# Optimization experiments

Hardware: AMD Instinct MI355X
Metric: run time of the kernel (lower is better)

Reference implementation:

```python
import jax, jax.numpy as jnp
import numpy as np

GROUP_SIZE = 128

def dequantize(imatrix, scales, zeros, group_size, out_dtype):
    # repeat group-wise scales/zeros along axis 0 to full weight shape
    rs = jnp.repeat(scales, group_size, axis=0)
    rz = jnp.repeat(zeros, group_size, axis=0)
    return ((imatrix.astype(rs.dtype) - rz.astype(rs.dtype)) * rs).astype(out_dtype)

def setup_inputs() -> dict:
    key = jax.random.key(0)
    ks = jax.random.split(key, 10)
    H, I, G = 4096, 14336, GROUP_SIZE
    B, S = 4, 2048
    x = jax.random.normal(ks[0], (B, S, H), dtype=jnp.float32)
    gate_w = jax.random.randint(ks[1], (H, I), 0, 16, dtype=jnp.int32)
    gate_z = jax.random.randint(ks[2], (H // G, I), 0, 16, dtype=jnp.int32)
    gate_s = jax.random.uniform(ks[3], (H // G, I), dtype=jnp.float32) * 0.01
    up_w = jax.random.randint(ks[4], (H, I), 0, 16, dtype=jnp.int32)
    up_z = jax.random.randint(ks[5], (H // G, I), 0, 16, dtype=jnp.int32)
    up_s = jax.random.uniform(ks[6], (H // G, I), dtype=jnp.float32) * 0.01
    down_w = jax.random.randint(ks[7], (I, H), 0, 16, dtype=jnp.int32)
    down_z = jax.random.randint(ks[8], (I // G, H), 0, 16, dtype=jnp.int32)
    down_s = jax.random.uniform(ks[9], (I // G, H), dtype=jnp.float32) * 0.01
    return {"x": x, "gate_w": gate_w, "gate_z": gate_z, "gate_s": gate_s,
            "up_w": up_w, "up_z": up_z, "up_s": up_s,
            "down_w": down_w, "down_z": down_z, "down_s": down_s}

def reference(x, gate_w, gate_z, gate_s, up_w, up_z, up_s, down_w, down_z, down_s):
    dt = x.dtype
    gate_proj = dequantize(gate_w, gate_s, gate_z, GROUP_SIZE, dt)  # [H, I]
    up_proj = dequantize(up_w, up_s, up_z, GROUP_SIZE, dt)          # [H, I]
    down_proj = dequantize(down_w, down_s, down_z, GROUP_SIZE, dt)  # [I, H]
    gate = jax.nn.silu(jnp.dot(x, gate_proj))  # [B, S, I]
    up = jnp.dot(x, up_proj)                   # [B, S, I]
    return jnp.dot(gate * up, down_proj)       # [B, S, H]
```

## Files before the change

### kernel.cpp

```cpp
#include <hip/hip_runtime.h>
#include <cstdint>
#include <cstddef>

typedef unsigned short u16;
typedef unsigned int u32;
typedef float f32x4 __attribute__((ext_vector_type(4)));
typedef __bf16 bf16x8 __attribute__((ext_vector_type(8)));

__device__ inline u16 f32_to_bf16(float f) {
  u32 u = __float_as_uint(f);
  u = (u + 0x7FFFu + ((u >> 16) & 1u)) >> 16;
  return (u16)u;
}

#define GLD16(src, dst)                                                        \
  __builtin_amdgcn_global_load_lds(                                            \
      (const __attribute__((address_space(1))) u32*)(src),                     \
      (__attribute__((address_space(3))) u32*)(dst), 16, 0, 0)

__device__ inline void stage_tile(const char* gbase, long stride_b, u16* tile,
                                  int tid) {
  const int wave = tid >> 6, lane = tid & 63;
  const int wbase = wave * 4096;
#pragma unroll
  for (int c = 0; c < 4; ++c) {
    const int d = wbase + c * 1024 + lane * 16;
    const int row = d >> 7;
    const int off = d & 127;
    const int kb = off ^ ((row & 7) << 4);
    const char* src = gbase + (long)row * stride_b + kb;
    char* dst = (char*)tile + wbase + c * 1024;
    GLD16(src, dst);
  }
}

__device__ inline bf16x8 frag_ld(const u16* tile, int row, int ks, int p) {
  const int byte = row * 128 + (((ks << 6) + (p << 4)) ^ ((row & 7) << 4));
  return *(const bf16x8*)((const char*)tile + byte);
}

__global__ void k_convert_x(const float* __restrict__ x, u16* __restrict__ o) {
  const long i = (long)blockIdx.x * 256 + threadIdx.x;
  const float4 a = ((const float4*)x)[i * 2];
  const float4 b = ((const float4*)x)[i * 2 + 1];
  uint4 r;
  r.x = (u32)f32_to_bf16(a.x) | ((u32)f32_to_bf16(a.y) << 16);
  r.y = (u32)f32_to_bf16(a.z) | ((u32)f32_to_bf16(a.w) << 16);
  r.z = (u32)f32_to_bf16(b.x) | ((u32)f32_to_bf16(b.y) << 16);
  r.w = (u32)f32_to_bf16(b.z) | ((u32)f32_to_bf16(b.w) << 16);
  ((uint4*)o)[i] = r;
}

__global__ __launch_bounds__(256) void k_dequant(const int* __restrict__ W,
                                                 const int* __restrict__ Z,
                                                 const float* __restrict__ S,
                                                 u16* __restrict__ out, int K,
                                                 int N) {
  __shared__ u16 ldsT[256 * 66];
  const int k0 = blockIdx.x * 64, n0 = blockIdx.y * 256;
  const int t = threadIdx.x;
  const int n4 = t & 63;
  const int kr = t >> 6;
  const int g = k0 >> 7;
  const int nb = n0 + n4 * 4;
  const int4 z4 = *(const int4*)(Z + (size_t)g * N + nb);
  const float4 s4 = *(const float4*)(S + (size_t)g * N + nb);
#pragma unroll
  for (int pass = 0; pass < 16; ++pass) {
    const int kl = kr + pass * 4;
    const int4 w4 = *(const int4*)(W + (size_t)(k0 + kl) * N + nb);
    ldsT[(n4 * 4 + 0) * 66 + kl] = f32_to_bf16((float)(w4.x - z4.x) * s4.x);
    ldsT[(n4 * 4 + 1) * 66 + kl] = f32_to_bf16((float)(w4.y - z4.y) * s4.y);
    ldsT[(n4 * 4 + 2) * 66 + kl] = f32_to_bf16((float)(w4.z - z4.z) * s4.z);
    ldsT[(n4 * 4 + 3) * 66 + kl] = f32_to_bf16((float)(w4.w - z4.w) * s4.w);
  }
  __syncthreads();
#pragma unroll
  for (int pass = 0; pass < 8; ++pass) {
    const int nl = pass * 32 + (t >> 3);
    const int kc = (t & 7) * 8;
    const u16* p = &ldsT[nl * 66 + kc];
    const u32 w0 = *(const u32*)(p + 0);
    const u32 w1 = *(const u32*)(p + 2);
    const u32 w2 = *(const u32*)(p + 4);
    const u32 w3 = *(const u32*)(p + 6);
    *(uint4*)(out + (size_t)(n0 + nl) * K + k0 + kc) =
        make_uint4(w0, w1, w2, w3);
  }
}

__global__ __launch_bounds__(256, 2) void k_gemm_gu(
    const u16* __restrict__ X, const u16* __restrict__ WG,
    const u16* __restrict__ WU, u16* __restrict__ Hout) {
  __shared__ u16 lA[128 * 64], lG[128 * 64], lU[128 * 64];
  const int m0 = blockIdx.x * 128, n0 = blockIdx.y * 128;
  const int tid = threadIdx.x, lane = tid & 63, p = lane >> 4, r16 = lane & 15;
  const int wave = tid >> 6, wr = wave >> 1, wc = wave & 1;

  f32x4 aG[4][4], aU[4][4];
  const f32x4 zero = {0.f, 0.f, 0.f, 0.f};
#pragma unroll
  for (int i = 0; i < 4; ++i)
#pragma unroll
    for (int j = 0; j < 4; ++j) {
      aG[i][j] = zero;
      aU[i][j] = zero;
    }

  const char* xb = (const char*)(X + (size_t)m0 * 4096);
  const char* gb = (const char*)(WG + (size_t)n0 * 4096);
  const char* ub = (const char*)(WU + (size_t)n0 * 4096);

  for (int kt = 0; kt < 64; ++kt) {
    const int kb = kt * 128;
    stage_tile(xb + kb, 8192, lA, tid);
    stage_tile(gb + kb, 8192, lG, tid);
    stage_tile(ub + kb, 8192, lU, tid);
    __syncthreads();
#pragma unroll
    for (int ks = 0; ks < 2; ++ks) {
      bf16x8 af[4], gf[4], uf[4];
#pragma unroll
      for (int i = 0; i < 4; ++i)
        af[i] = frag_ld(lA, wr * 64 + i * 16 + r16, ks, p);
#pragma unroll
      for (int j = 0; j < 4; ++j) {
        gf[j] = frag_ld(lG, wc * 64 + j * 16 + r16, ks, p);
        uf[j] = frag_ld(lU, wc * 64 + j * 16 + r16, ks, p);
      }
#pragma unroll
      for (int i = 0; i < 4; ++i)
#pragma unroll
        for (int j = 0; j < 4; ++j) {
          aG[i][j] = __builtin_amdgcn_mfma_f32_16x16x32_bf16(af[i], gf[j],
                                                             aG[i][j], 0, 0, 0);
          aU[i][j] = __builtin_amdgcn_mfma_f32_16x16x32_bf16(af[i], uf[j],
                                                             aU[i][j], 0, 0, 0);
        }
    }
    __syncthreads();
  }
#pragma unroll
  for (int i = 0; i < 4; ++i) {
    const int row = m0 + wr * 64 + i * 16 + p * 4;
#pragma unroll
    for (int j = 0; j < 4; ++j) {
      const int col = n0 + wc * 64 + j * 16 + r16;
      u16* dst = Hout + (size_t)row * 14336 + col;
#pragma unroll
      for (int r = 0; r < 4; ++r) {
        const float gv = aG[i][j][r], uv = aU[i][j][r];
        const float sv = gv / (1.f + __expf(-gv)) * uv;
        dst[(size_t)r * 14336] = f32_to_bf16(sv);
      }
    }
  }
}

__global__ __launch_bounds__(256, 2) void k_gemm_down(
    const u16* __restrict__ Hin, const u16* __restrict__ WD,
    float* __restrict__ Out) {
  __shared__ u16 lA[128 * 64], lB[128 * 64];
  const int m0 = blockIdx.x * 128, n0 = blockIdx.y * 128;
  const int tid = threadIdx.x, lane = tid & 63, p = lane >> 4, r16 = lane & 15;
  const int wave = tid >> 6, wr = wave >> 1, wc = wave & 1;

  f32x4 acc[4][4];
  const f32x4 zero = {0.f, 0.f, 0.f, 0.f};
#pragma unroll
  for (int i = 0; i < 4; ++i)
#pragma unroll
    for (int j = 0; j < 4; ++j) acc[i][j] = zero;

  const char* ab = (const char*)(Hin + (size_t)m0 * 14336);
  const char* bb = (const char*)(WD + (size_t)n0 * 14336);

  for (int kt = 0; kt < 224; ++kt) {
    const long kb = (long)kt * 128;
    stage_tile(ab + kb, 28672, lA, tid);
    stage_tile(bb + kb, 28672, lB, tid);
    __syncthreads();
#pragma unroll
    for (int ks = 0; ks < 2; ++ks) {
      bf16x8 af[4], bf[4];
#pragma unroll
      for (int i = 0; i < 4; ++i)
        af[i] = frag_ld(lA, wr * 64 + i * 16 + r16, ks, p);
#pragma unroll
      for (int j = 0; j < 4; ++j)
        bf[j] = frag_ld(lB, wc * 64 + j * 16 + r16, ks, p);
#pragma unroll
      for (int i = 0; i < 4; ++i)
#pragma unroll
        for (int j = 0; j < 4; ++j)
          acc[i][j] = __builtin_amdgcn_mfma_f32_16x16x32_bf16(
              af[i], bf[j], acc[i][j], 0, 0, 0);
    }
    __syncthreads();
  }
#pragma unroll
  for (int i = 0; i < 4; ++i) {
    const int row = m0 + wr * 64 + i * 16 + p * 4;
#pragma unroll
    for (int j = 0; j < 4; ++j) {
      const int col = n0 + wc * 64 + j * 16 + r16;
      float* dst = Out + (size_t)row * 4096 + col;
#pragma unroll
      for (int r = 0; r < 4; ++r) dst[(size_t)r * 4096] = acc[i][j][r];
    }
  }
}

__global__ void k_fill(float* o, long n, float v) {
  const long i = (long)blockIdx.x * 256 + threadIdx.x;
  if (i < n) o[i] = v;
}

extern "C" void kernel_launch(void* const* d_in, const int* in_sizes, int n_in,
                              void* d_out, int out_size, void* d_ws,
                              size_t ws_size, hipStream_t stream) {
  const float* x = (const float*)d_in[0];
  const int* gw = (const int*)d_in[1];
  const int* gz = (const int*)d_in[2];
  const float* gs = (const float*)d_in[3];
  const int* uw = (const int*)d_in[4];
  const int* uz = (const int*)d_in[5];
  const float* us = (const float*)d_in[6];
  const int* dw = (const int*)d_in[7];
  const int* dz = (const int*)d_in[8];
  const float* dsc = (const float*)d_in[9];
  float* out = (float*)d_out;

  const size_t NX = 33554432UL, NW = 58720256UL, NH = 117440512UL;
  const size_t need = 2UL * (NX + 3UL * NW + NH);
  if (ws_size < need) {
    k_fill<<<(out_size + 255) / 256, 256, 0, stream>>>(out, out_size, 1.0e6f);
    return;
  }
  u16* wsx = (u16*)d_ws;
  u16* wgq = wsx + NX;
  u16* wuq = wgq + NW;
  u16* wdq = wuq + NW;
  u16* wh = wdq + NW;

  k_convert_x<<<16384, 256, 0, stream>>>(x, wsx);
  dim3 dq1(64, 56);
  k_dequant<<<dq1, 256, 0, stream>>>(gw, gz, gs, wgq, 4096, 14336);
  k_dequant<<<dq1, 256, 0, stream>>>(uw, uz, us, wuq, 4096, 14336);
  dim3 dq2(224, 16);
  k_dequant<<<dq2, 256, 0, stream>>>(dw, dz, dsc, wdq, 14336, 4096);
  dim3 g1(64, 112);
  k_gemm_gu<<<g1, 256, 0, stream>>>(wsx, wgq, wuq, wh);
  dim3 g2(64, 32);
  k_gemm_down<<<g2, 256, 0, stream>>>(wh, wdq, out);
}
```

Baseline: 2.831 ms.

## Pipeline both GEMMs with double-buffered LDS, larger tiles, and 8-wave ping-pong

Rewrites the gate/up and down GEMM kernels to use 512-thread blocks with larger tiles (256x128 and 256x256). The LDS is split into K-halves and double-buffered, with async global-to-LDS loads issued two tiles ahead, so loads overlap MFMA work instead of stalling on a syncthreads each iteration. Barriers and s_setprio interleave the load issue with the MFMA bursts. In exchange there is more LDS per block and more accumulator registers, which may lower occupancy, and the manual vmcnt accounting is fragile.

```diff
diff --git a/kernel.cpp b/kernel.cpp
--- a/kernel.cpp
+++ b/kernel.cpp
@@ -18,25 +18,26 @@
       (const __attribute__((address_space(1))) u32*)(src),                     \
       (__attribute__((address_space(3))) u32*)(dst), 16, 0, 0)
 
-__device__ inline void stage_tile(const char* gbase, long stride_b, u16* tile,
-                                  int tid) {
-  const int wave = tid >> 6, lane = tid & 63;
-  const int wbase = wave * 4096;
-#pragma unroll
-  for (int c = 0; c < 4; ++c) {
-    const int d = wbase + c * 1024 + lane * 16;
-    const int row = d >> 7;
-    const int off = d & 127;
-    const int kb = off ^ ((row & 7) << 4);
-    const char* src = gbase + (long)row * stride_b + kb;
-    char* dst = (char*)tile + wbase + c * 1024;
-    GLD16(src, dst);
-  }
-}
-
-__device__ inline bf16x8 frag_ld(const u16* tile, int row, int ks, int p) {
-  const int byte = row * 128 + (((ks << 6) + (p << 4)) ^ ((row & 7) << 4));
-  return *(const bf16x8*)((const char*)tile + byte);
+#define SBAR() __builtin_amdgcn_s_barrier()
+#define SETPRIO(x) __builtin_amdgcn_s_setprio(x)
+#define WAIT_LGKM0()                                                           \
+  do {                                                                         \
+    asm volatile("s_waitcnt lgkmcnt(0)" ::: "memory");                         \
+    __builtin_amdgcn_sched_barrier(0);                                         \
+  } while (0)
+#define MFMA16(a, b, c) __builtin_amdgcn_mfma_f32_16x16x32_bf16(a, b, c, 0, 0, 0)
+
+__device__ inline void stage_one(const char* laneBase, long colByte,
+                                 long strideB, int rowBase, u16* ldsHalf,
+                                 int wave) {
+  const char* src = laneBase + colByte + (long)rowBase * strideB;
+  char* dst = (char*)ldsHalf + rowBase * 64 + wave * 1024;
+  GLD16(src, dst);
+}
+
+__device__ inline bf16x8 fragK(const u16* half, int row, int p) {
+  const int byte = row * 64 + (((p ^ row) & 3) << 4);
+  return *(const bf16x8*)((const char*)half + byte);
 }
 
 __global__ void k_convert_x(const float* __restrict__ x, u16* __restrict__ o) {
@@ -89,63 +90,110 @@
   }
 }
 
-__global__ __launch_bounds__(256, 2) void k_gemm_gu(
+__global__ __launch_bounds__(512, 2) void k_gemm_gu(
     const u16* __restrict__ X, const u16* __restrict__ WG,
     const u16* __restrict__ WU, u16* __restrict__ Hout) {
-  __shared__ u16 lA[128 * 64], lG[128 * 64], lU[128 * 64];
-  const int m0 = blockIdx.x * 128, n0 = blockIdx.y * 128;
-  const int tid = threadIdx.x, lane = tid & 63, p = lane >> 4, r16 = lane & 15;
-  const int wave = tid >> 6, wr = wave >> 1, wc = wave & 1;
-
-  f32x4 aG[4][4], aU[4][4];
+  __shared__ __align__(16) u16 lA[2][2][8192];
+  __shared__ __align__(16) u16 lG[2][2][4096];
+  __shared__ __align__(16) u16 lU[2][2][4096];
+  const int NKT = 64;
+  const int m0 = blockIdx.x * 256, n0 = blockIdx.y * 128;
+  const int tid = threadIdx.x, lane = tid & 63, wave = tid >> 6;
+  const int p = lane >> 4, r16 = lane & 15;
+  const int wr = wave >> 2, wc = wave & 3;
+
+  const int srow = wave * 16 + (lane >> 2);
+  const int kb = (((lane & 3) ^ (lane >> 2)) & 3) << 4;
+  const char* baA = (const char*)X + (long)(m0 + srow) * 8192 + kb;
+  const char* baG = (const char*)WG + (long)(n0 + srow) * 8192 + kb;
+  const char* baU = (const char*)WU + (long)(n0 + srow) * 8192 + kb;
+
+#define ISS_A(kts, ksh, rb) \
+  stage_one(baA, (long)(kts)*128 + (ksh)*64, 8192, rb, &lA[(kts)&1][ksh][0], wave)
+#define ISS_G(kts, ksh) \
+  stage_one(baG, (long)(kts)*128 + (ksh)*64, 8192, 0, &lG[(kts)&1][ksh][0], wave)
+#define ISS_U(kts, ksh) \
+  stage_one(baU, (long)(kts)*128 + (ksh)*64, 8192, 0, &lU[(kts)&1][ksh][0], wave)
+
+  f32x4 aG[8][2], aU[8][2];
   const f32x4 zero = {0.f, 0.f, 0.f, 0.f};
 #pragma unroll
-  for (int i = 0; i < 4; ++i)
-#pragma unroll
-    for (int j = 0; j < 4; ++j) {
+  for (int i = 0; i < 8; ++i)
+#pragma unroll
+    for (int j = 0; j < 2; ++j) {
       aG[i][j] = zero;
       aU[i][j] = zero;
     }
 
-  const char* xb = (const char*)(X + (size_t)m0 * 4096);
-  const char* gb = (const char*)(WG + (size_t)n0 * 4096);
-  const char* ub = (const char*)(WU + (size_t)n0 * 4096);
-
-  for (int kt = 0; kt < 64; ++kt) {
-    const int kb = kt * 128;
-    stage_tile(xb + kb, 8192, lA, tid);
-    stage_tile(gb + kb, 8192, lG, tid);
-    stage_tile(ub + kb, 8192, lU, tid);
-    __syncthreads();
-#pragma unroll
-    for (int ks = 0; ks < 2; ++ks) {
-      bf16x8 af[4], gf[4], uf[4];
-#pragma unroll
-      for (int i = 0; i < 4; ++i)
-        af[i] = frag_ld(lA, wr * 64 + i * 16 + r16, ks, p);
-#pragma unroll
-      for (int j = 0; j < 4; ++j) {
-        gf[j] = frag_ld(lG, wc * 64 + j * 16 + r16, ks, p);
-        uf[j] = frag_ld(lU, wc * 64 + j * 16 + r16, ks, p);
-      }
-#pragma unroll
-      for (int i = 0; i < 4; ++i)
-#pragma unroll
-        for (int j = 0; j < 4; ++j) {
-          aG[i][j] = __builtin_amdgcn_mfma_f32_16x16x32_bf16(af[i], gf[j],
-                                                             aG[i][j], 0, 0, 0);
-          aU[i][j] = __builtin_amdgcn_mfma_f32_16x16x32_bf16(af[i], uf[j],
-                                                             aU[i][j], 0, 0, 0);
-        }
-    }
-    __syncthreads();
-  }
-#pragma unroll
-  for (int i = 0; i < 4; ++i) {
-    const int row = m0 + wr * 64 + i * 16 + p * 4;
-#pragma unroll
-    for (int j = 0; j < 4; ++j) {
-      const int col = n0 + wc * 64 + j * 16 + r16;
+  ISS_A(0, 0, 0); ISS_A(0, 0, 128); ISS_G(0, 0); ISS_U(0, 0);
+  ISS_A(0, 1, 0); ISS_A(0, 1, 128); ISS_G(0, 1); ISS_U(0, 1);
+  ISS_A(1, 0, 0); ISS_A(1, 0, 128); ISS_G(1, 0); ISS_U(1, 0);
+  ISS_A(1, 1, 0); ISS_A(1, 1, 128);
+  asm volatile("s_waitcnt vmcnt(6)" ::: "memory");
+  SBAR();
+
+  for (int kt = 0; kt < NKT; ++kt) {
+    const int b = kt & 1;
+    const bool g1 = (kt + 1 < NKT), g2 = (kt + 2 < NKT);
+#pragma unroll
+    for (int ksh = 0; ksh < 2; ++ksh) {
+      bf16x8 af[8], gf[2], uf[2];
+      const u16* hA = &lA[b][ksh][0];
+      const u16* hG = &lG[b][ksh][0];
+      const u16* hU = &lU[b][ksh][0];
+#pragma unroll
+      for (int i = 0; i < 8; ++i)
+        af[i] = fragK(hA, wr * 128 + i * 16 + r16, p);
+#pragma unroll
+      for (int j = 0; j < 2; ++j) {
+        gf[j] = fragK(hG, wc * 32 + j * 16 + r16, p);
+        uf[j] = fragK(hU, wc * 32 + j * 16 + r16, p);
+      }
+      if (ksh == 0) {
+        if (g1) { ISS_G(kt + 1, 1); ISS_U(kt + 1, 1); }
+      } else {
+        if (g2) { ISS_G(kt + 2, 0); ISS_U(kt + 2, 0); }
+      }
+      SBAR();
+      WAIT_LGKM0();
+      SETPRIO(1);
+#pragma unroll
+      for (int i = 0; i < 8; ++i)
+#pragma unroll
+        for (int j = 0; j < 2; ++j) aG[i][j] = MFMA16(af[i], gf[j], aG[i][j]);
+      SETPRIO(0);
+      SBAR();
+      if (ksh == 0) {
+        if (g2) { ISS_A(kt + 2, 0, 0); ISS_A(kt + 2, 0, 128); }
+      } else {
+        if (g2) { ISS_A(kt + 2, 1, 0); ISS_A(kt + 2, 1, 128); }
+      }
+      SBAR();
+      SETPRIO(1);
+#pragma unroll
+      for (int i = 0; i < 8; ++i)
+#pragma unroll
+        for (int j = 0; j < 2; ++j) aU[i][j] = MFMA16(af[i], uf[j], aU[i][j]);
+      SETPRIO(0);
+      if (ksh == 1) {
+        if (kt < NKT - 2)
+          asm volatile("s_waitcnt vmcnt(6)" ::: "memory");
+        else if (kt == NKT - 2)
+          asm volatile("s_waitcnt vmcnt(0)" ::: "memory");
+      }
+      SBAR();
+    }
+  }
+#undef ISS_A
+#undef ISS_G
+#undef ISS_U
+
+#pragma unroll
+  for (int i = 0; i < 8; ++i) {
+    const int row = m0 + wr * 128 + i * 16 + p * 4;
+#pragma unroll
+    for (int j = 0; j < 2; ++j) {
+      const int col = n0 + wc * 32 + j * 16 + r16;
       u16* dst = Hout + (size_t)row * 14336 + col;
 #pragma unroll
       for (int r = 0; r < 4; ++r) {
@@ -157,50 +205,98 @@
   }
 }
 
-__global__ __launch_bounds__(256, 2) void k_gemm_down(
+__global__ __launch_bounds__(512, 2) void k_gemm_down(
     const u16* __restrict__ Hin, const u16* __restrict__ WD,
     float* __restrict__ Out) {
-  __shared__ u16 lA[128 * 64], lB[128 * 64];
-  const int m0 = blockIdx.x * 128, n0 = blockIdx.y * 128;
-  const int tid = threadIdx.x, lane = tid & 63, p = lane >> 4, r16 = lane & 15;
-  const int wave = tid >> 6, wr = wave >> 1, wc = wave & 1;
-
-  f32x4 acc[4][4];
+  __shared__ __align__(16) u16 lA[2][2][8192];
+  __shared__ __align__(16) u16 lB[2][2][8192];
+  const int NKT = 224;
+  const int m0 = blockIdx.x * 256, n0 = blockIdx.y * 256;
+  const int tid = threadIdx.x, lane = tid & 63, wave = tid >> 6;
+  const int p = lane >> 4, r16 = lane & 15;
+  const int wr = wave >> 2, wc = wave & 3;
+
+  const int srow = wave * 16 + (lane >> 2);
+  const int kb = (((lane & 3) ^ (lane >> 2)) & 3) << 4;
+  const char* baA = (const char*)Hin + (long)(m0 + srow) * 28672 + kb;
+  const char* baB = (const char*)WD + (long)(n0 + srow) * 28672 + kb;
+
+#define ISS_A(kts, ksh, rb) \
+  stage_one(baA, (long)(kts)*128 + (ksh)*64, 28672, rb, &lA[(kts)&1][ksh][0], wave)
+#define ISS_B(kts, ksh, rb) \
+  stage_one(baB, (long)(kts)*128 + (ksh)*64, 28672, rb, &lB[(kts)&1][ksh][0], wave)
+
+  f32x4 acc[8][4];
   const f32x4 zero = {0.f, 0.f, 0.f, 0.f};
 #pragma unroll
-  for (int i = 0; i < 4; ++i)
+  for (int i = 0; i < 8; ++i)
 #pragma unroll
     for (int j = 0; j < 4; ++j) acc[i][j] = zero;
 
-  const char* ab = (const char*)(Hin + (size_t)m0 * 14336);
-  const char* bb = (const char*)(WD + (size_t)n0 * 14336);
-
-  for (int kt = 0; kt < 224; ++kt) {
-    const long kb = (long)kt * 128;
-    stage_tile(ab + kb, 28672, lA, tid);
-    stage_tile(bb + kb, 28672, lB, tid);
-    __syncthreads();
-#pragma unroll
-    for (int ks = 0; ks < 2; ++ks) {
-      bf16x8 af[4], bf[4];
-#pragma unroll
-      for (int i = 0; i < 4; ++i)
-        af[i] = frag_ld(lA, wr * 64 + i * 16 + r16, ks, p);
+  ISS_A(0, 0, 0); ISS_A(0, 0, 128); ISS_B(0, 0, 0); ISS_B(0, 0, 128);
+  ISS_A(0, 1, 0); ISS_A(0, 1, 128); ISS_B(0, 1, 0); ISS_B(0, 1, 128);
+  ISS_A(1, 0, 0); ISS_A(1, 0, 128); ISS_B(1, 0, 0); ISS_B(1, 0, 128);
+  ISS_A(1, 1, 0); ISS_A(1, 1, 128);
+  asm volatile("s_waitcnt vmcnt(6)" ::: "memory");
+  SBAR();
+
+  for (int kt = 0; kt < NKT; ++kt) {
+    const int b = kt & 1;
+    const bool g1 = (kt + 1 < NKT), g2 = (kt + 2 < NKT);
+#pragma unroll
+    for (int ksh = 0; ksh < 2; ++ksh) {
+      bf16x8 af[8], bfr[4];
+      const u16* hA = &lA[b][ksh][0];
+      const u16* hB = &lB[b][ksh][0];
+#pragma unroll
+      for (int i = 0; i < 8; ++i)
+        af[i] = fragK(hA, wr * 128 + i * 16 + r16, p);
 #pragma unroll
       for (int j = 0; j < 4; ++j)
-        bf[j] = frag_ld(lB, wc * 64 + j * 16 + r16, ks, p);
-#pragma unroll
-      for (int i = 0; i < 4; ++i)
-#pragma unroll
-        for (int j = 0; j < 4; ++j)
-          acc[i][j] = __builtin_amdgcn_mfma_f32_16x16x32_bf16(
-              af[i], bf[j], acc[i][j], 0, 0, 0);
-    }
-    __syncthreads();
-  }
-#pragma unroll
-  for (int i = 0; i < 4; ++i) {
-    const int row = m0 + wr * 64 + i * 16 + p * 4;
+        bfr[j] = fragK(hB, wc * 64 + j * 16 + r16, p);
+      if (ksh == 0) {
+        if (g1) { ISS_B(kt + 1, 1, 0); ISS_B(kt + 1, 1, 128); }
+      } else {
+        if (g2) { ISS_B(kt + 2, 0, 0); ISS_B(kt + 2, 0, 128); }
+      }
+      SBAR();
+      WAIT_LGKM0();
+      SETPRIO(1);
+#pragma unroll
+      for (int i = 0; i < 8; ++i)
+#pragma unroll
+        for (int j = 0; j < 2; ++j)
+          acc[i][j] = MFMA16(af[i], bfr[j], acc[i][j]);
+      SETPRIO(0);
+      SBAR();
+      if (ksh == 0) {
+        if (g2) { ISS_A(kt + 2, 0, 0); ISS_A(kt + 2, 0, 128); }
+      } else {
+        if (g2) { ISS_A(kt + 2, 1, 0); ISS_A(kt + 2, 1, 128); }
+      }
+      SBAR();
+      SETPRIO(1);
+#pragma unroll
+      for (int i = 0; i < 8; ++i)
+#pragma unroll
+        for (int j = 2; j < 4; ++j)
+          acc[i][j] = MFMA16(af[i], bfr[j], acc[i][j]);
+      SETPRIO(0);
+      if (ksh == 1) {
+        if (kt < NKT - 2)
+          asm volatile("s_waitcnt vmcnt(6)" ::: "memory");
+        else if (kt == NKT - 2)
+          asm volatile("s_waitcnt vmcnt(0)" ::: "memory");
+      }
+      SBAR();
+    }
+  }
+#undef ISS_A
+#undef ISS_B
+
+#pragma unroll
+  for (int i = 0; i < 8; ++i) {
+    const int row = m0 + wr * 128 + i * 16 + p * 4;
 #pragma unroll
     for (int j = 0; j < 4; ++j) {
       const int col = n0 + wc * 64 + j * 16 + r16;
@@ -231,8 +327,8 @@
   const float* dsc = (const float*)d_in[9];
   float* out = (float*)d_out;
 
-  const size_t NX = 33554432UL, NW = 58720256UL, NH = 117440512UL;
-  const size_t need = 2UL * (NX + 3UL * NW + NH);
+  const size_t NX = 33554432UL, NW = 58720256UL;
+  const size_t need = 2UL * (NX + 3UL * NW + 117440512UL);
   if (ws_size < need) {
     k_fill<<<(out_size + 255) / 256, 256, 0, stream>>>(out, out_size, 1.0e6f);
     return;
@@ -249,8 +345,8 @@
   k_dequant<<<dq1, 256, 0, stream>>>(uw, uz, us, wuq, 4096, 14336);
   dim3 dq2(224, 16);
   k_dequant<<<dq2, 256, 0, stream>>>(dw, dz, dsc, wdq, 14336, 4096);
-  dim3 g1(64, 112);
-  k_gemm_gu<<<g1, 256, 0, stream>>>(wsx, wgq, wuq, wh);
-  dim3 g2(64, 32);
-  k_gemm_down<<<g2, 256, 0, stream>>>(wh, wdq, out);
-}
+  dim3 g1(32, 112);
+  k_gemm_gu<<<g1, 512, 0, stream>>>(wsx, wgq, wuq, wh);
+  dim3 g2(32, 16);
+  k_gemm_down<<<g2, 512, 0, stream>>>(wh, wdq, out);
+}
```

Result: slower. 3.629 ms (+28.2%).
